# Optimization experiments

Measured on AMD Instinct MI355X. Metric: run time of the kernel, lower is better.

## Reference

```python
import jax, jax.numpy as jnp
import numpy as np

HIDDEN = 2304
N_HEADS = 8
N_KV = 4
HEAD_DIM = 256
WINDOW = 1024
SOFTCAP = 50.0
EPS = 1e-6
SCALING = HEAD_DIM ** -0.5  # (head_dim * query_pre_attn_scalar=1.0) ** -0.5


def _rotate_half(x):
    d = x.shape[-1] // 2
    return jnp.concatenate([-x[..., d:], x[..., :d]], axis=-1)


def setup_inputs() -> dict:
    key = jax.random.key(0)
    ks = jax.random.split(key, 8)
    B, S = 2, 2048
    hidden_states = jax.random.normal(ks[0], (B, S, HIDDEN), dtype=jnp.float32)
    # RoPE tables, theta=10000
    inv_freq = 1.0 / (10000.0 ** (jnp.arange(0, HEAD_DIM, 2, dtype=jnp.float32) / HEAD_DIM))
    pos = jnp.arange(S, dtype=jnp.float32)
    freqs = pos[:, None] * inv_freq[None, :]              # [S, D/2]
    emb = jnp.concatenate([freqs, freqs], axis=-1)        # [S, D]
    cos = jnp.broadcast_to(jnp.cos(emb)[None], (B, S, HEAD_DIM)).astype(jnp.float32)
    sin = jnp.broadcast_to(jnp.sin(emb)[None], (B, S, HEAD_DIM)).astype(jnp.float32)
    std = 0.02
    rms_weight = jax.random.normal(ks[1], (HIDDEN,), dtype=jnp.float32) * std
    Wq = jax.random.normal(ks[2], (N_HEADS * HEAD_DIM, HIDDEN), dtype=jnp.float32) * std
    Wk = jax.random.normal(ks[3], (N_KV * HEAD_DIM, HIDDEN), dtype=jnp.float32) * std
    Wv = jax.random.normal(ks[4], (N_KV * HEAD_DIM, HIDDEN), dtype=jnp.float32) * std
    Wo = jax.random.normal(ks[5], (HIDDEN, N_HEADS * HEAD_DIM), dtype=jnp.float32) * std
    return {"hidden_states": hidden_states, "cos": cos, "sin": sin,
            "rms_weight": rms_weight, "Wq": Wq, "Wk": Wk, "Wv": Wv, "Wo": Wo}


def reference(hidden_states, cos, sin, rms_weight, Wq, Wk, Wv, Wo):
    B, S, H = hidden_states.shape
    # Gemma2 RMSNorm: x * rsqrt(mean(x^2)+eps) * (1 + w), computed in fp32
    xf = hidden_states.astype(jnp.float32)
    norm = xf * jax.lax.rsqrt(jnp.mean(xf * xf, axis=-1, keepdims=True) + EPS)
    x = (norm * (1.0 + rms_weight)).astype(hidden_states.dtype)

    q = jnp.einsum('bsh,dh->bsd', x, Wq).reshape(B, S, N_HEADS, HEAD_DIM).transpose(0, 2, 1, 3)
    k = jnp.einsum('bsh,dh->bsd', x, Wk).reshape(B, S, N_KV, HEAD_DIM).transpose(0, 2, 1, 3)
    v = jnp.einsum('bsh,dh->bsd', x, Wv).reshape(B, S, N_KV, HEAD_DIM).transpose(0, 2, 1, 3)

    c = cos[:, None, :, :]  # [B,1,S,D]
    s = sin[:, None, :, :]
    q = q * c + _rotate_half(q) * s
    k = k * c + _rotate_half(k) * s

    groups = N_HEADS // N_KV
    k = jnp.repeat(k, groups, axis=1)  # [B,Hq,S,D]
    v = jnp.repeat(v, groups, axis=1)

    scores = jnp.einsum('bhqd,bhkd->bhqk', q, k) * SCALING
    scores = SOFTCAP * jnp.tanh(scores / SOFTCAP)

    i = jnp.arange(S)[:, None]
    j = jnp.arange(S)[None, :]
    allowed = (j <= i) & ((i - j) < WINDOW)  # causal + sliding window
    scores = jnp.where(allowed[None, None], scores, jnp.float32(-1e30))

    w = jax.nn.softmax(scores.astype(jnp.float32), axis=-1).astype(q.dtype)
    attn = jnp.einsum('bhqk,bhkd->bhqd', w, v)
    attn = attn.transpose(0, 2, 1, 3).reshape(B, S, N_HEADS * HEAD_DIM)
    out = jnp.einsum('bsd,hd->bsh', attn, Wo)
    return hidden_states + out
```

## Files before the change

### kernel.cpp

```cpp
#include <hip/hip_runtime.h>
#include <cstdint>

typedef __bf16 bf16;
typedef __bf16 bf16x8 __attribute__((ext_vector_type(8)));
typedef __bf16 bf16x4 __attribute__((ext_vector_type(4)));
typedef float  f32x4  __attribute__((ext_vector_type(4)));

#define HIDDEN 2304
#define NQ 2048
#define NKV 1024
#define SEQ 2048

typedef __attribute__((address_space(1))) void gv_t;
typedef __attribute__((address_space(3))) void lv_t;
__device__ __forceinline__ void gld16(const void* g, void* l) {
  __builtin_amdgcn_global_load_lds((gv_t*)g, (lv_t*)l, 16, 0, 0);
}

#define BAR()    asm volatile("s_barrier" ::: "memory")
#define LGKM(n)  asm volatile("s_waitcnt lgkmcnt(" #n ")" ::: "memory")
#define VM6()    asm volatile("s_waitcnt vmcnt(6)" ::: "memory")
#define VM2()    asm volatile("s_waitcnt vmcnt(2)" ::: "memory")
#define VM0()    asm volatile("s_waitcnt vmcnt(0)" ::: "memory")
#define SCHED0() __builtin_amdgcn_sched_barrier(0)

__global__ __launch_bounds__(256) void rmsnorm_kernel(const float* __restrict__ x,
                                                      const float* __restrict__ w,
                                                      bf16* __restrict__ xb) {
  const int row = blockIdx.x, t = threadIdx.x;
  const float* xr = x + (size_t)row * HIDDEN;
  float v[9]; float ss = 0.f;
#pragma unroll
  for (int i = 0; i < 9; ++i) { v[i] = xr[t + i * 256]; ss += v[i] * v[i]; }
#pragma unroll
  for (int o = 32; o; o >>= 1) ss += __shfl_xor(ss, o, 64);
  __shared__ float wss[4];
  if ((t & 63) == 0) wss[t >> 6] = ss;
  __syncthreads();
  ss = wss[0] + wss[1] + wss[2] + wss[3];
  const float rs = rsqrtf(ss * (1.0f / HIDDEN) + 1e-6f);
  bf16* xo = xb + (size_t)row * HIDDEN;
#pragma unroll
  for (int i = 0; i < 9; ++i) xo[t + i * 256] = (bf16)(v[i] * rs * (1.0f + w[t + i * 256]));
}

#define NW0 (2048 * 2304)
#define NW1 (1024 * 2304)
#define NW3 (2304 * 2048)
__global__ __launch_bounds__(256) void cvt4_kernel(const float* __restrict__ s0, const float* __restrict__ s1,
                                                   const float* __restrict__ s2, const float* __restrict__ s3,
                                                   bf16* __restrict__ d0, bf16* __restrict__ d1,
                                                   bf16* __restrict__ d2, bf16* __restrict__ d3) {
  int i = (blockIdx.x * 256 + threadIdx.x) * 4;
  const float* s; bf16* d;
  if (i < NW0) { s = s0; d = d0; }
  else if (i < NW0 + NW1) { s = s1; d = d1; i -= NW0; }
  else if (i < NW0 + 2 * NW1) { s = s2; d = d2; i -= NW0 + NW1; }
  else { s = s3; d = d3; i -= NW0 + 2 * NW1; }
  const float4 f = *(const float4*)(s + i);
  bf16x4 o; o.x = (bf16)f.x; o.y = (bf16)f.y; o.z = (bf16)f.z; o.w = (bf16)f.w;
  *(bf16x4*)(d + i) = o;
}

__global__ __launch_bounds__(256) void rope_kernel(bf16* __restrict__ q, bf16* __restrict__ k,
                                                   const float* __restrict__ cosb,
                                                   const float* __restrict__ sinb) {
  const int tid = blockIdx.x * 256 + threadIdx.x;
  const int QN = 4096 * 8 * 128;
  const int KN = 4096 * 4 * 128;
  bf16* p; int row, d;
  if (tid < QN) {
    row = tid >> 10; const int rem = tid & 1023; d = rem & 127;
    p = q + (size_t)row * NQ + (rem >> 7) * 256 + d;
  } else {
    const int t2 = tid - QN; if (t2 >= KN) return;
    row = t2 >> 9; const int rem = t2 & 511; d = rem & 127;
    p = k + (size_t)row * NKV + (rem >> 7) * 256 + d;
  }
  const size_t cb = (size_t)row * 256 + d;
  const float c0 = cosb[cb], s0 = sinb[cb], c1 = cosb[cb + 128], s1 = sinb[cb + 128];
  const float a = (float)p[0], b = (float)p[128];
  p[0]   = (bf16)(a * c0 - b * s0);
  p[128] = (bf16)(b * c1 + a * s1);
}

__device__ __forceinline__ void stage_half(const char* gbase, int stride, char* ldshalf, int tid) {
  const int c2 = ((tid & 7) * 16) ^ (((tid >> 3) & 7) << 4);
#pragma unroll
  for (int q = 0; q < 2; ++q) {
    const int r = q * 64 + (tid >> 3);
    gld16(gbase + (size_t)r * stride + c2, ldshalf + q * 8192 + tid * 16);
  }
}

template<int MH, int NH, int KS>
__device__ __forceinline__ void mfma_burst(const bf16x8 (&af)[4][2], const bf16x8 (&bn)[2][2],
                                           f32x4 (&acc)[8][4]) {
  __builtin_amdgcn_s_setprio(1);
#pragma unroll
  for (int m = 0; m < 4; ++m)
#pragma unroll
    for (int n = 0; n < 2; ++n)
      acc[MH * 4 + m][NH * 2 + n] =
          __builtin_amdgcn_mfma_f32_16x16x32_bf16(af[m][KS], bn[n][KS], acc[MH * 4 + m][NH * 2 + n], 0, 0, 0);
  __builtin_amdgcn_s_setprio(0);
}

template<int NT, int NY, int MODE>
__global__ __launch_bounds__(512) void gemm8p(const bf16* __restrict__ A, const bf16* __restrict__ B,
                                              bf16* __restrict__ Cq, bf16* __restrict__ Ck,
                                              bf16* __restrict__ Cvt, float* __restrict__ fo,
                                              const float* __restrict__ resid, int Nd) {
  __shared__ char lds[131072];
  const int Ks = NT * 128;
  const char* Aby = (const char*)A;
  const char* Bby = (const char*)B;

  int wg = blockIdx.x;
  const int chunk = (int)gridDim.x >> 3;
  wg = (wg & 7) * chunk + (wg >> 3);
  const int by = wg % NY, bx = wg / NY;
  const int m0 = bx * 256, n0 = by * 256;

  const int tid = threadIdx.x, lane = tid & 63, wv = tid >> 6;
  const int wm = wv >> 2, wn = wv & 3;
  const int r16 = lane & 15, g = lane >> 4;
  const int xr = (r16 & 7) << 4;
  const int cb0 = (g * 16) ^ xr, cb1 = (64 + g * 16) ^ xr;
  const int rdA = wm * 16384 + r16 * 128;
  const int rdB = 32768 + (wn >> 1) * 16384 + (wn & 1) * 8192 + r16 * 128;

  const char* A0g = Aby + (size_t)m0 * Ks;
  const char* A1g = Aby + (size_t)(m0 + 128) * Ks;
  const char* B0g = Bby + (size_t)n0 * Ks;
  const char* B1g = Bby + (size_t)(n0 + 128) * Ks;

  f32x4 acc[8][4] = {};
  bf16x8 a0[4][2], a1[4][2], bb01[2][2], bb23[2][2];

  auto read_a0bb01 = [&](const char* buf) {
#pragma unroll
    for (int n = 0; n < 2; ++n) bb01[n][0] = *(const bf16x8*)(buf + rdB + n * 2048 + cb0);
#pragma unroll
    for (int n = 0; n < 2; ++n) bb01[n][1] = *(const bf16x8*)(buf + rdB + n * 2048 + cb1);
#pragma unroll
    for (int m = 0; m < 4; ++m) a0[m][0] = *(const bf16x8*)(buf + rdA + m * 2048 + cb0);
#pragma unroll
    for (int m = 0; m < 4; ++m) a0[m][1] = *(const bf16x8*)(buf + rdA + m * 2048 + cb1);
  };

  stage_half(A0g, Ks, lds + 0,     tid);
  stage_half(A1g, Ks, lds + 16384, tid);
  stage_half(B0g, Ks, lds + 32768, tid);
  stage_half(B1g, Ks, lds + 49152, tid);
  stage_half(B0g + 128, Ks, lds + 65536 + 32768, tid);
  stage_half(A0g + 128, Ks, lds + 65536 + 0,     tid);
  stage_half(A1g + 128, Ks, lds + 65536 + 16384, tid);
  VM6(); BAR();
  read_a0bb01(lds);

  for (int t = 0; t < NT; ++t) {
    const char* bufc = lds + (size_t)(t & 1) * 65536;
    char* bufn = lds + (size_t)((t + 1) & 1) * 65536;
    char* bufs = lds + (size_t)(t & 1) * 65536;
    LGKM(0);
#pragma unroll
    for (int n = 0; n < 2; ++n) bb23[n][0] = *(const bf16x8*)(bufc + rdB + (2 + n) * 2048 + cb0);
#pragma unroll
    for (int n = 0; n < 2; ++n) bb23[n][1] = *(const bf16x8*)(bufc + rdB + (2 + n) * 2048 + cb1);
#pragma unroll
    for (int m = 0; m < 4; ++m) a1[m][0] = *(const bf16x8*)(bufc + rdA + 8192 + m * 2048 + cb0);
#pragma unroll
    for (int m = 0; m < 4; ++m) a1[m][1] = *(const bf16x8*)(bufc + rdA + 8192 + m * 2048 + cb1);
    SCHED0();
    mfma_burst<0, 0, 0>(a0, bb01, acc);
    mfma_burst<0, 0, 1>(a0, bb01, acc);
    SCHED0(); BAR();
    LGKM(8);
    if (t + 1 < NT)
      stage_half(B1g + (size_t)(t + 1) * 128, Ks, bufn + 49152, tid);
    SCHED0();
    mfma_burst<0, 1, 0>(a0, bb23, acc);
    mfma_burst<0, 1, 1>(a0, bb23, acc);
    SCHED0(); BAR();
    LGKM(0);
    if (t + 2 < NT)
      stage_half(B0g + (size_t)(t + 2) * 128, Ks, bufs + 32768, tid);
    SCHED0();
    mfma_burst<1, 0, 0>(a1, bb01, acc);
    mfma_burst<1, 0, 1>(a1, bb01, acc);
    SCHED0(); BAR();
    if (t < NT - 2) { VM2(); } else if (t == NT - 2) { VM0(); }
    if (t + 2 < NT) {
      stage_half(A0g + (size_t)(t + 2) * 128, Ks, bufs + 0,     tid);
      stage_half(A1g + (size_t)(t + 2) * 128, Ks, bufs + 16384, tid);
    }
    SCHED0();
    mfma_burst<1, 1, 0>(a1, bb23, acc);
    mfma_burst<1, 1, 1>(a1, bb23, acc);
    SCHED0(); BAR();
    if (t + 1 < NT) read_a0bb01(bufn);
  }

  const int mrow = m0 + wm * 128 + g * 4;
  const int ncol = n0 + wn * 64 + r16;
#pragma unroll
  for (int i = 0; i < 8; ++i)
#pragma unroll
    for (int j = 0; j < 4; ++j)
#pragma unroll
      for (int e = 0; e < 4; ++e) {
        const int m = mrow + i * 16 + e;
        const int n = ncol + j * 16;
        const float vv = acc[i][j][e];
        if constexpr (MODE == 0) {
          if (n0 < 2048) {
            Cq[(size_t)m * 2048 + n] = (bf16)vv;
          } else if (n0 < 3072) {
            Ck[(size_t)m * 1024 + (n - 2048)] = (bf16)vv;
          } else {
            const int b2 = m >> 11, s = m & 2047;
            Cvt[((size_t)b2 * 1024 + (n - 3072)) * SEQ + s] = (bf16)vv;
          }
        } else {
          fo[(size_t)m * Nd + n] = vv + resid[(size_t)m * Nd + n];
        }
      }
}

__device__ __forceinline__ void attn_load(const bf16* __restrict__ kgp, const bf16* __restrict__ vgp,
                                          int j0, int t, bf16x8* kr, bf16x8* vr) {
#pragma unroll
  for (int it = 0; it < 4; ++it) {
    const int flat = it * 2048 + t * 8;
    kr[it] = *(const bf16x8*)&kgp[(size_t)((flat >> 8) + j0) * NKV + (flat & 255)];
    vr[it] = *(const bf16x8*)&vgp[(size_t)(flat >> 5) * SEQ + j0 + (flat & 31)];
  }
}

__global__ __launch_bounds__(256) void attn_kernel(const bf16* __restrict__ q, const bf16* __restrict__ k,
                                                   const bf16* __restrict__ vt, bf16* __restrict__ ao) {
  __shared__ bf16 smem[21248];
  bf16* const qs  = smem;
  bf16* const ksl = smem;
  bf16* const vtl = smem + 8448;
  bf16* const pl  = smem + 18688;
  int qt = blockIdx.x;
  const int h = blockIdx.y, b = blockIdx.z;
  if (b) qt = 31 - qt;
  const int kvh = h >> 1;
  const int t = threadIdx.x, lane = t & 63, w = t >> 6;
  const int r16 = lane & 15, g = lane >> 4;
  const int i_base = qt * 64;

  {
    const bf16* qg = q + ((size_t)(b * SEQ + i_base)) * NQ + h * 256;
#pragma unroll
    for (int it = 0; it < 8; ++it) {
      const int flat = it * 2048 + t * 8;
      const int row = flat >> 8, dd = flat & 255;
      *(bf16x8*)&qs[row * 264 + dd] = *(const bf16x8*)&qg[(size_t)row * NQ + dd];
    }
  }
  __syncthreads();
  bf16x8 aq[8];
#pragma unroll
  for (int c = 0; c < 8; ++c) aq[c] = *(const bf16x8*)&qs[(w * 16 + r16) * 264 + c * 32 + g * 8];

  f32x4 oacc[16] = {};
  float lrun[4] = {0.f, 0.f, 0.f, 0.f};
  int jb = i_base - 1023; if (jb < 0) jb = 0; jb &= ~31;
  const int je = i_base + 63;
  const bf16* kg = k + (size_t)b * SEQ * NKV + kvh * 256;
  const bf16* vg = vt + ((size_t)b * NKV + kvh * 256) * SEQ;

  bf16x8 kr[4], vr[4];
  attn_load(kg, vg, jb, t, kr, vr);

  for (int j0 = jb; j0 <= je; j0 += 32) {
    __syncthreads();
#pragma unroll
    for (int it = 0; it < 4; ++it) {
      const int flat = it * 2048 + t * 8;
      *(bf16x8*)&ksl[(flat >> 8) * 264 + (flat & 255)] = kr[it];
      *(bf16x8*)&vtl[(flat >> 5) * 40 + (flat & 31)] = vr[it];
    }
    __syncthreads();
    const int jn = (j0 + 32 <= je) ? (j0 + 32) : j0;
    attn_load(kg, vg, jn, t, kr, vr);

    f32x4 sc0 = {}, sc1 = {};
#pragma unroll
    for (int c = 0; c < 8; ++c) {
      const bf16x8 b0 = *(const bf16x8*)&ksl[r16 * 264 + c * 32 + g * 8];
      const bf16x8 b1 = *(const bf16x8*)&ksl[(16 + r16) * 264 + c * 32 + g * 8];
      sc0 = __builtin_amdgcn_mfma_f32_16x16x32_bf16(aq[c], b0, sc0, 0, 0, 0);
      sc1 = __builtin_amdgcn_mfma_f32_16x16x32_bf16(aq[c], b1, sc1, 0, 0, 0);
    }
    const bool full = (j0 + 31 <= i_base) && (i_base + 63 - j0 < 1024);
#pragma unroll
    for (int e = 0; e < 4; ++e) {
      const float t0 = __expf(sc0[e] * 0.0025f);
      const float t1 = __expf(sc1[e] * 0.0025f);
      float p0 = __expf(-100.0f / (t0 + 1.0f));
      float p1 = __expf(-100.0f / (t1 + 1.0f));
      if (!full) {
        const int irow = i_base + w * 16 + g * 4 + e;
        const int jg0 = j0 + r16, jg1 = j0 + 16 + r16;
        if (jg0 > irow || irow - jg0 >= 1024) p0 = 0.f;
        if (jg1 > irow || irow - jg1 >= 1024) p1 = 0.f;
      }
      const bf16 b0 = (bf16)p0, b1 = (bf16)p1;
      lrun[e] += (float)b0 + (float)b1;
      pl[w * 640 + (g * 4 + e) * 40 + r16] = b0;
      pl[w * 640 + (g * 4 + e) * 40 + 16 + r16] = b1;
    }
    const bf16x8 pa = *(const bf16x8*)&pl[w * 640 + r16 * 40 + g * 8];
#pragma unroll
    for (int nf = 0; nf < 16; ++nf) {
      const bf16x8 vb = *(const bf16x8*)&vtl[(nf * 16 + r16) * 40 + g * 8];
      oacc[nf] = __builtin_amdgcn_mfma_f32_16x16x32_bf16(pa, vb, oacc[nf], 0, 0, 0);
    }
  }
  float inv[4];
#pragma unroll
  for (int e = 0; e < 4; ++e) {
#pragma unroll
    for (int o = 1; o < 16; o <<= 1) lrun[e] += __shfl_xor(lrun[e], o, 64);
    inv[e] = 1.0f / lrun[e];
  }
  bf16* aor = ao + ((size_t)(b * SEQ + i_base + w * 16)) * NQ + h * 256;
#pragma unroll
  for (int nf = 0; nf < 16; ++nf)
#pragma unroll
    for (int e = 0; e < 4; ++e)
      aor[(size_t)(g * 4 + e) * NQ + nf * 16 + r16] = (bf16)(oacc[nf][e] * inv[e]);
}

extern "C" void kernel_launch(void* const* d_in, const int* in_sizes, int n_in,
                              void* d_out, int out_size, void* d_ws, size_t ws_size,
                              hipStream_t stream) {
  const float* hs   = (const float*)d_in[0];
  const float* cosb = (const float*)d_in[1];
  const float* sinb = (const float*)d_in[2];
  const float* rw   = (const float*)d_in[3];
  const float* Wq   = (const float*)d_in[4];
  const float* Wk   = (const float*)d_in[5];
  const float* Wv   = (const float*)d_in[6];
  const float* Wo   = (const float*)d_in[7];
  float* out = (float*)d_out;
  char* ws = (char*)d_ws;

  bf16* xb   = (bf16*)(ws);
  bf16* wqkv = (bf16*)(ws + 18874368);
  bf16* wkb  = wqkv + (size_t)2048 * 2304;
  bf16* wvb  = wqkv + (size_t)3072 * 2304;
  bf16* wob  = (bf16*)(ws + 37748736);
  bf16* qg   = (bf16*)(ws + 47185920);
  bf16* kg   = (bf16*)(ws + 63963136);
  bf16* vtg  = (bf16*)(ws + 72351744);
  bf16* ag   = (bf16*)(ws + 80740352);

  rmsnorm_kernel<<<4096, 256, 0, stream>>>(hs, rw, xb);
  cvt4_kernel<<<(NW0 + 2 * NW1 + NW3) / 4 / 256, 256, 0, stream>>>(Wq, Wk, Wv, Wo, wqkv, wkb, wvb, wob);
  gemm8p<36, 16, 0><<<256, 512, 0, stream>>>(xb, wqkv, qg, kg, vtg, nullptr, nullptr, 4096);
  rope_kernel<<<(4096 * 8 * 128 + 4096 * 4 * 128) / 256, 256, 0, stream>>>(qg, kg, cosb, sinb);
  attn_kernel<<<dim3(32, 8, 2), 256, 0, stream>>>(qg, kg, vtg, ag);
  gemm8p<32, 9, 1><<<144, 512, 0, stream>>>(ag, wob, nullptr, nullptr, nullptr, out, hs, 2304);
}
```

Measured before the change: 259.9 us.

## Replace output projection GEMM with 128x128-tile kernel and XCD-aware block remap

Adds a new 128x128-tile, 256-thread GEMM for the output projection, launched as 576 workgroups instead of 144 larger-tile ones. Operand loads go straight to LDS into a swizzled, double-buffered layout, with loads and MFMA quarters interleaved under priority hints. Blocks are remapped across the eight XCD chunks. The aim is better occupancy across the 256 CUs, in exchange for less reuse per tile and more global traffic.

```diff
diff --git a/kernel.cpp b/kernel.cpp
--- a/kernel.cpp
+++ b/kernel.cpp
@@ -19,6 +19,7 @@
 
 #define BAR()    asm volatile("s_barrier" ::: "memory")
 #define LGKM(n)  asm volatile("s_waitcnt lgkmcnt(" #n ")" ::: "memory")
+#define VM8()    asm volatile("s_waitcnt vmcnt(8)" ::: "memory")
 #define VM6()    asm volatile("s_waitcnt vmcnt(6)" ::: "memory")
 #define VM2()    asm volatile("s_waitcnt vmcnt(2)" ::: "memory")
 #define VM0()    asm volatile("s_waitcnt vmcnt(0)" ::: "memory")
@@ -228,6 +229,127 @@
       }
 }
 
+__device__ __forceinline__ void stage128(const char* gbase, int KsB, char* dst, int tid) {
+#pragma unroll
+  for (int it = 0; it < 4; ++it) {
+    const int o = it * 4096 + tid * 16;
+    const int r = o >> 7, c = o & 127;
+    gld16(gbase + (size_t)r * KsB + (c ^ ((r & 7) << 4)), dst + o);
+  }
+}
+
+template<int NT>
+__global__ __launch_bounds__(256) void gemm8p128(const bf16* __restrict__ A, const bf16* __restrict__ B,
+                                                 float* __restrict__ fo, const float* __restrict__ resid) {
+  __shared__ char lds[65536];
+  const int Ks = NT * 128;
+  const char* Aby = (const char*)A;
+  const char* Bby = (const char*)B;
+
+  int wg = blockIdx.x;
+  const int chunk = (int)gridDim.x >> 3;
+  wg = (wg & 7) * chunk + (wg >> 3);
+  const int bx = wg / 18, by = wg % 18;
+  const int m0 = bx * 128, n0 = by * 128;
+
+  const int tid = threadIdx.x, lane = tid & 63, wv = tid >> 6;
+  const int wm = wv >> 1, wn = wv & 1;
+  const int r16 = lane & 15, g = lane >> 4;
+  const int xr = (r16 & 7) << 4;
+  const int cb0 = (g * 16) ^ xr, cb1 = (64 + g * 16) ^ xr;
+  const int rdA = (wm * 64 + r16) * 128;
+  const int rdB = 16384 + (wn * 64 + r16) * 128;
+
+  const char* Ag = Aby + (size_t)m0 * Ks;
+  const char* Bg = Bby + (size_t)n0 * Ks;
+
+  f32x4 acc[4][4] = {};
+  bf16x8 a01[2][2], a23[2][2], b01[2][2], b23[2][2];
+
+  stage128(Ag,       Ks, lds + 0,             tid);
+  stage128(Bg,       Ks, lds + 16384,         tid);
+  stage128(Ag + 128, Ks, lds + 32768 + 0,     tid);
+  stage128(Bg + 128, Ks, lds + 32768 + 16384, tid);
+  VM8(); BAR();
+
+  for (int t = 0; t < NT; ++t) {
+    const char* bufc = lds + (size_t)(t & 1) * 32768;
+    char* bufs = lds + (size_t)(t & 1) * 32768;
+#pragma unroll
+    for (int m = 0; m < 2; ++m) {
+      a01[m][0] = *(const bf16x8*)(bufc + rdA + m * 2048 + cb0);
+      a01[m][1] = *(const bf16x8*)(bufc + rdA + m * 2048 + cb1);
+      b01[m][0] = *(const bf16x8*)(bufc + rdB + m * 2048 + cb0);
+      b01[m][1] = *(const bf16x8*)(bufc + rdB + m * 2048 + cb1);
+    }
+    __builtin_amdgcn_s_setprio(1);
+#pragma unroll
+    for (int m = 0; m < 2; ++m)
+#pragma unroll
+      for (int n = 0; n < 2; ++n) {
+        acc[m][n] = __builtin_amdgcn_mfma_f32_16x16x32_bf16(a01[m][0], b01[n][0], acc[m][n], 0, 0, 0);
+        acc[m][n] = __builtin_amdgcn_mfma_f32_16x16x32_bf16(a01[m][1], b01[n][1], acc[m][n], 0, 0, 0);
+      }
+    __builtin_amdgcn_s_setprio(0);
+#pragma unroll
+    for (int n = 0; n < 2; ++n) {
+      b23[n][0] = *(const bf16x8*)(bufc + rdB + (2 + n) * 2048 + cb0);
+      b23[n][1] = *(const bf16x8*)(bufc + rdB + (2 + n) * 2048 + cb1);
+    }
+    __builtin_amdgcn_s_setprio(1);
+#pragma unroll
+    for (int m = 0; m < 2; ++m)
+#pragma unroll
+      for (int n = 0; n < 2; ++n) {
+        acc[m][2 + n] = __builtin_amdgcn_mfma_f32_16x16x32_bf16(a01[m][0], b23[n][0], acc[m][2 + n], 0, 0, 0);
+        acc[m][2 + n] = __builtin_amdgcn_mfma_f32_16x16x32_bf16(a01[m][1], b23[n][1], acc[m][2 + n], 0, 0, 0);
+      }
+    __builtin_amdgcn_s_setprio(0);
+    BAR();
+    if (t + 2 < NT) stage128(Bg + (size_t)(t + 2) * 128, Ks, bufs + 16384, tid);
+#pragma unroll
+    for (int m = 0; m < 2; ++m) {
+      a23[m][0] = *(const bf16x8*)(bufc + rdA + (2 + m) * 2048 + cb0);
+      a23[m][1] = *(const bf16x8*)(bufc + rdA + (2 + m) * 2048 + cb1);
+    }
+    __builtin_amdgcn_s_setprio(1);
+#pragma unroll
+    for (int m = 0; m < 2; ++m)
+#pragma unroll
+      for (int n = 0; n < 2; ++n) {
+        acc[2 + m][n] = __builtin_amdgcn_mfma_f32_16x16x32_bf16(a23[m][0], b01[n][0], acc[2 + m][n], 0, 0, 0);
+        acc[2 + m][n] = __builtin_amdgcn_mfma_f32_16x16x32_bf16(a23[m][1], b01[n][1], acc[2 + m][n], 0, 0, 0);
+      }
+    __builtin_amdgcn_s_setprio(0);
+    BAR();
+    if (t + 2 < NT) stage128(Ag + (size_t)(t + 2) * 128, Ks, bufs + 0, tid);
+    __builtin_amdgcn_s_setprio(1);
+#pragma unroll
+    for (int m = 0; m < 2; ++m)
+#pragma unroll
+      for (int n = 0; n < 2; ++n) {
+        acc[2 + m][2 + n] = __builtin_amdgcn_mfma_f32_16x16x32_bf16(a23[m][0], b23[n][0], acc[2 + m][2 + n], 0, 0, 0);
+        acc[2 + m][2 + n] = __builtin_amdgcn_mfma_f32_16x16x32_bf16(a23[m][1], b23[n][1], acc[2 + m][2 + n], 0, 0, 0);
+      }
+    __builtin_amdgcn_s_setprio(0);
+    if (t + 2 < NT) { VM8(); } else if (t == NT - 2) { VM0(); }
+    BAR();
+  }
+
+  const int mrow = m0 + wm * 64 + g * 4;
+  const int ncol = n0 + wn * 64 + r16;
+#pragma unroll
+  for (int i = 0; i < 4; ++i)
+#pragma unroll
+    for (int j = 0; j < 4; ++j)
+#pragma unroll
+      for (int e = 0; e < 4; ++e) {
+        const int m = mrow + i * 16 + e;
+        const int n = ncol + j * 16;
+        fo[(size_t)m * 2304 + n] = acc[i][j][e] + resid[(size_t)m * 2304 + n];
+      }
+}
+
 __device__ __forceinline__ void attn_load(const bf16* __restrict__ kgp, const bf16* __restrict__ vgp,
                                           int j0, int t, bf16x8* kr, bf16x8* vr) {
 #pragma unroll
@@ -366,5 +488,5 @@
   gemm8p<36, 16, 0><<<256, 512, 0, stream>>>(xb, wqkv, qg, kg, vtg, nullptr, nullptr, 4096);
   rope_kernel<<<(4096 * 8 * 128 + 4096 * 4 * 128) / 256, 256, 0, stream>>>(qg, kg, cosb, sinb);
   attn_kernel<<<dim3(32, 8, 2), 256, 0, stream>>>(qg, kg, vtg, ag);
-  gemm8p<32, 9, 1><<<144, 512, 0, stream>>>(ag, wob, nullptr, nullptr, nullptr, out, hs, 2304);
-}
+  gemm8p128<32><<<576, 256, 0, stream>>>(ag, wob, out, hs);
+}
```

New measurement: 260.8 us. Within noise of the previous version (+0.3%).

## Split-K the output projection GEMM with a separate bf16 partial reduction

Applied to the files above, without the earlier changes.

Replaces the 144-block output projection GEMM with a split-K (2-way) 128x128-tile GEMM launched over 1152 blocks, writing bf16 partial sums into a workspace region, followed by a reduce kernel that adds the partials and the residual. The aim is to fill more of the GPU's compute units than 144 blocks can. In exchange it adds an extra pass of partial-sum traffic and a kernel launch. The new GEMM uses simple synchronous LDS loads without the pipelining of the old kernel. Storing partials in bf16 also loses some precision.

```diff
diff --git a/kernel.cpp b/kernel.cpp
--- a/kernel.cpp
+++ b/kernel.cpp
@@ -228,6 +228,73 @@
       }
 }
 
+__global__ __launch_bounds__(256) void gemmsk(const bf16* __restrict__ A, const bf16* __restrict__ B,
+                                              bf16* __restrict__ P) {
+  __shared__ bf16 As[128][72];
+  __shared__ bf16 Bs[128][72];
+  const int t = threadIdx.x, lane = t & 63, w = t >> 6;
+  const int wr = w >> 1, wc = w & 1;
+  const int r16 = lane & 15, g = lane >> 4;
+  int wg = blockIdx.x;
+  wg = (wg & 7) * 144 + (wg >> 3);
+  const int bx = wg % 32, rem = wg / 32;
+  const int by = rem % 18, kz = rem / 18;
+  const int m0 = bx * 128, n0 = by * 128;
+  const int kbeg = kz * 1024, kend = kbeg + 1024;
+  f32x4 acc[4][4] = {};
+  for (int k0 = kbeg; k0 < kend; k0 += 64) {
+    __syncthreads();
+#pragma unroll
+    for (int it = 0; it < 4; ++it) {
+      const int flat = it * 2048 + t * 8;
+      const int row = flat >> 6, kk = flat & 63;
+      *(bf16x8*)&As[row][kk] = *(const bf16x8*)&A[(size_t)(m0 + row) * 2048 + k0 + kk];
+      *(bf16x8*)&Bs[row][kk] = *(const bf16x8*)&B[(size_t)(n0 + row) * 2048 + k0 + kk];
+    }
+    __syncthreads();
+#pragma unroll
+    for (int ks = 0; ks < 2; ++ks) {
+      bf16x8 af[4], bfv[4];
+#pragma unroll
+      for (int i = 0; i < 4; ++i) {
+        af[i]  = *(const bf16x8*)&As[wr * 64 + i * 16 + r16][ks * 32 + g * 8];
+        bfv[i] = *(const bf16x8*)&Bs[wc * 64 + i * 16 + r16][ks * 32 + g * 8];
+      }
+#pragma unroll
+      for (int i = 0; i < 4; ++i)
+#pragma unroll
+        for (int j = 0; j < 4; ++j)
+          acc[i][j] = __builtin_amdgcn_mfma_f32_16x16x32_bf16(af[i], bfv[j], acc[i][j], 0, 0, 0);
+    }
+  }
+  bf16* pp = P + (size_t)kz * 4096 * 2304;
+#pragma unroll
+  for (int i = 0; i < 4; ++i)
+#pragma unroll
+    for (int j = 0; j < 4; ++j) {
+      const int mb = m0 + wr * 64 + i * 16 + g * 4;
+      const int n = n0 + wc * 64 + j * 16 + r16;
+#pragma unroll
+      for (int e = 0; e < 4; ++e)
+        pp[(size_t)(mb + e) * 2304 + n] = (bf16)acc[i][j][e];
+    }
+}
+
+__global__ __launch_bounds__(256) void reduce_kernel(const bf16* __restrict__ P,
+                                                     const float* __restrict__ hs,
+                                                     float* __restrict__ out) {
+  const int i = (blockIdx.x * 256 + threadIdx.x) * 4;
+  const bf16x4 p0 = *(const bf16x4*)&P[i];
+  const bf16x4 p1 = *(const bf16x4*)&P[9437184 + i];
+  const float4 h = *(const float4*)&hs[i];
+  float4 o;
+  o.x = (float)p0.x + (float)p1.x + h.x;
+  o.y = (float)p0.y + (float)p1.y + h.y;
+  o.z = (float)p0.z + (float)p1.z + h.z;
+  o.w = (float)p0.w + (float)p1.w + h.w;
+  *(float4*)&out[i] = o;
+}
+
 __device__ __forceinline__ void attn_load(const bf16* __restrict__ kgp, const bf16* __restrict__ vgp,
                                           int j0, int t, bf16x8* kr, bf16x8* vr) {
 #pragma unroll
@@ -360,11 +427,13 @@
   bf16* kg   = (bf16*)(ws + 63963136);
   bf16* vtg  = (bf16*)(ws + 72351744);
   bf16* ag   = (bf16*)(ws + 80740352);
+  bf16* part = (bf16*)(ws);
 
   rmsnorm_kernel<<<4096, 256, 0, stream>>>(hs, rw, xb);
   cvt4_kernel<<<(NW0 + 2 * NW1 + NW3) / 4 / 256, 256, 0, stream>>>(Wq, Wk, Wv, Wo, wqkv, wkb, wvb, wob);
   gemm8p<36, 16, 0><<<256, 512, 0, stream>>>(xb, wqkv, qg, kg, vtg, nullptr, nullptr, 4096);
   rope_kernel<<<(4096 * 8 * 128 + 4096 * 4 * 128) / 256, 256, 0, stream>>>(qg, kg, cosb, sinb);
   attn_kernel<<<dim3(32, 8, 2), 256, 0, stream>>>(qg, kg, vtg, ag);
-  gemm8p<32, 9, 1><<<144, 512, 0, stream>>>(ag, wob, nullptr, nullptr, nullptr, out, hs, 2304);
-}
+  gemmsk<<<1152, 256, 0, stream>>>(ag, wob, part);
+  reduce_kernel<<<9216, 256, 0, stream>>>(part, hs, out);
+}
```

Result: slower. 283.3 us (+9.0%).

## Fuse RoPE into QKV GEMM epilogue via interleaved weight row permutation

Applied to the files above, without the earlier changes.

Permutes the Wq/Wk weight rows during bf16 conversion so that each rotate-half pair (d, d+128) lands in adjacent output columns. The QKV GEMM epilogue then applies RoPE with a lane shuffle and cos/sin loads, and writes back in the original head-dim order. This removes the separate rope kernel launch and its read-modify-write pass over Q and K. In exchange, the epilogue gains extra global cos/sin loads and the weight conversion does integer division per element.

```diff
diff --git a/kernel.cpp b/kernel.cpp
--- a/kernel.cpp
+++ b/kernel.cpp
@@ -52,36 +52,22 @@
                                                    bf16* __restrict__ d0, bf16* __restrict__ d1,
                                                    bf16* __restrict__ d2, bf16* __restrict__ d3) {
   int i = (blockIdx.x * 256 + threadIdx.x) * 4;
-  const float* s; bf16* d;
-  if (i < NW0) { s = s0; d = d0; }
-  else if (i < NW0 + NW1) { s = s1; d = d1; i -= NW0; }
-  else if (i < NW0 + 2 * NW1) { s = s2; d = d2; i -= NW0 + NW1; }
-  else { s = s3; d = d3; i -= NW0 + 2 * NW1; }
+  const float* s; bf16* dst; size_t oidx;
+  if (i < NW0) {
+    s = s0; const int r = i / 2304, c = i % 2304, d = r & 255;
+    oidx = (size_t)((r & ~255) | ((d & 127) << 1) | (d >> 7)) * 2304 + c; dst = d0;
+  } else if (i < NW0 + NW1) {
+    i -= NW0;
+    s = s1; const int r = i / 2304, c = i % 2304, d = r & 255;
+    oidx = (size_t)((r & ~255) | ((d & 127) << 1) | (d >> 7)) * 2304 + c; dst = d1;
+  } else if (i < NW0 + 2 * NW1) {
+    i -= NW0 + NW1; s = s2; oidx = i; dst = d2;
+  } else {
+    i -= NW0 + 2 * NW1; s = s3; oidx = i; dst = d3;
+  }
   const float4 f = *(const float4*)(s + i);
   bf16x4 o; o.x = (bf16)f.x; o.y = (bf16)f.y; o.z = (bf16)f.z; o.w = (bf16)f.w;
-  *(bf16x4*)(d + i) = o;
-}
-
-__global__ __launch_bounds__(256) void rope_kernel(bf16* __restrict__ q, bf16* __restrict__ k,
-                                                   const float* __restrict__ cosb,
-                                                   const float* __restrict__ sinb) {
-  const int tid = blockIdx.x * 256 + threadIdx.x;
-  const int QN = 4096 * 8 * 128;
-  const int KN = 4096 * 4 * 128;
-  bf16* p; int row, d;
-  if (tid < QN) {
-    row = tid >> 10; const int rem = tid & 1023; d = rem & 127;
-    p = q + (size_t)row * NQ + (rem >> 7) * 256 + d;
-  } else {
-    const int t2 = tid - QN; if (t2 >= KN) return;
-    row = t2 >> 9; const int rem = t2 & 511; d = rem & 127;
-    p = k + (size_t)row * NKV + (rem >> 7) * 256 + d;
-  }
-  const size_t cb = (size_t)row * 256 + d;
-  const float c0 = cosb[cb], s0 = sinb[cb], c1 = cosb[cb + 128], s1 = sinb[cb + 128];
-  const float a = (float)p[0], b = (float)p[128];
-  p[0]   = (bf16)(a * c0 - b * s0);
-  p[128] = (bf16)(b * c1 + a * s1);
+  *(bf16x4*)(dst + oidx) = o;
 }
 
 __device__ __forceinline__ void stage_half(const char* gbase, int stride, char* ldshalf, int tid) {
@@ -110,7 +96,9 @@
 __global__ __launch_bounds__(512) void gemm8p(const bf16* __restrict__ A, const bf16* __restrict__ B,
                                               bf16* __restrict__ Cq, bf16* __restrict__ Ck,
                                               bf16* __restrict__ Cvt, float* __restrict__ fo,
-                                              const float* __restrict__ resid, int Nd) {
+                                              const float* __restrict__ resid, int Nd,
+                                              const float* __restrict__ cosb,
+                                              const float* __restrict__ sinb) {
   __shared__ char lds[131072];
   const int Ks = NT * 128;
   const char* Aby = (const char*)A;
@@ -212,18 +200,27 @@
       for (int e = 0; e < 4; ++e) {
         const int m = mrow + i * 16 + e;
         const int n = ncol + j * 16;
-        const float vv = acc[i][j][e];
+        float v = acc[i][j][e];
         if constexpr (MODE == 0) {
-          if (n0 < 2048) {
-            Cq[(size_t)m * 2048 + n] = (bf16)vv;
-          } else if (n0 < 3072) {
-            Ck[(size_t)m * 1024 + (n - 2048)] = (bf16)vv;
+          if (n0 < 3072) {
+            const float p = __shfl_xor(v, 1);
+            const int jj = n & 255;
+            const int f = jj >> 1;
+            const float c  = cosb[(size_t)m * 256 + f];
+            const float sn = sinb[(size_t)m * 256 + f];
+            v = (jj & 1) ? (v * c + p * sn) : (v * c - p * sn);
+            const int d = f + ((jj & 1) << 7);
+            if (n0 < 2048) {
+              Cq[(size_t)m * 2048 + (n & ~255) + d] = (bf16)v;
+            } else {
+              Ck[(size_t)m * 1024 + ((n - 2048) & ~255) + d] = (bf16)v;
+            }
           } else {
             const int b2 = m >> 11, s = m & 2047;
-            Cvt[((size_t)b2 * 1024 + (n - 3072)) * SEQ + s] = (bf16)vv;
+            Cvt[((size_t)b2 * 1024 + (n - 3072)) * SEQ + s] = (bf16)v;
           }
         } else {
-          fo[(size_t)m * Nd + n] = vv + resid[(size_t)m * Nd + n];
+          fo[(size_t)m * Nd + n] = v + resid[(size_t)m * Nd + n];
         }
       }
 }
@@ -363,8 +360,7 @@
 
   rmsnorm_kernel<<<4096, 256, 0, stream>>>(hs, rw, xb);
   cvt4_kernel<<<(NW0 + 2 * NW1 + NW3) / 4 / 256, 256, 0, stream>>>(Wq, Wk, Wv, Wo, wqkv, wkb, wvb, wob);
-  gemm8p<36, 16, 0><<<256, 512, 0, stream>>>(xb, wqkv, qg, kg, vtg, nullptr, nullptr, 4096);
-  rope_kernel<<<(4096 * 8 * 128 + 4096 * 4 * 128) / 256, 256, 0, stream>>>(qg, kg, cosb, sinb);
+  gemm8p<36, 16, 0><<<256, 512, 0, stream>>>(xb, wqkv, qg, kg, vtg, nullptr, nullptr, 4096, cosb, sinb);
   attn_kernel<<<dim3(32, 8, 2), 256, 0, stream>>>(qg, kg, vtg, ag);
-  gemm8p<32, 9, 1><<<144, 512, 0, stream>>>(ag, wob, nullptr, nullptr, nullptr, out, hs, 2304);
-}
+  gemm8p<32, 9, 1><<<144, 512, 0, stream>>>(ag, wob, nullptr, nullptr, nullptr, out, hs, 2304, nullptr, nullptr);
+}
```

Result: faster. 248.3 us (-4.5%).
